# Kernel tuning notes

Measured on AMD Instinct MI355X. Metric: run time of the kernel, lower is better.

Reference implementation:

```python
import jax, jax.numpy as jnp
import numpy as np

N_EMBD = 1024
N_HEAD = 16
HEAD_DIM = N_EMBD // N_HEAD
B, T = 2, 2048


def setup_inputs() -> dict:
    key = jax.random.key(0)
    ks = jax.random.split(key, 9)
    s = 1.0 / np.sqrt(N_EMBD)
    return {
        "x": jax.random.normal(ks[0], (B, T, N_EMBD), dtype=jnp.float32),
        "Wq": jax.random.normal(ks[1], (N_EMBD, N_EMBD), dtype=jnp.float32) * s,
        "bq": jax.random.normal(ks[2], (N_EMBD,), dtype=jnp.float32) * s,
        "Wk": jax.random.normal(ks[3], (N_EMBD, N_EMBD), dtype=jnp.float32) * s,
        "bk": jax.random.normal(ks[4], (N_EMBD,), dtype=jnp.float32) * s,
        "Wv": jax.random.normal(ks[5], (N_EMBD, N_EMBD), dtype=jnp.float32) * s,
        "bv": jax.random.normal(ks[6], (N_EMBD,), dtype=jnp.float32) * s,
        "Wp": jax.random.normal(ks[7], (N_EMBD, N_EMBD), dtype=jnp.float32) * s,
        "bp": jax.random.normal(ks[8], (N_EMBD,), dtype=jnp.float32) * s,
    }


def reference(x, Wq, bq, Wk, bk, Wv, bv, Wp, bp):
    b, t, c = x.shape
    # torch Linear: y = x @ W.T + b
    def proj(W, bias):
        y = jnp.einsum('btc,oc->bto', x, W) + bias
        return y.reshape(b, t, N_HEAD, HEAD_DIM).transpose(0, 2, 1, 3)  # [B,H,T,D]

    q = proj(Wq, bq)
    k = proj(Wk, bk)
    v = proj(Wv, bv)

    scale = 1.0 / np.sqrt(HEAD_DIM).astype(np.float32)
    scores = jnp.einsum('bhqd,bhkd->bhqk', q, k) * scale  # [B,H,T,T]
    causal = jnp.tril(jnp.ones((t, t), dtype=bool))
    scores = jnp.where(causal[None, None], scores, jnp.float32(-jnp.inf))
    attn = jax.nn.softmax(scores, axis=-1)
    out = jnp.einsum('bhqk,bhkd->bhqd', attn, v)  # [B,H,T,D]
    out = out.transpose(0, 2, 1, 3).reshape(b, t, c)
    out = jnp.einsum('btc,oc->bto', out, Wp) + bp
    return out
```

## Files before the change

kernel.cpp:

```cpp
#include <hip/hip_runtime.h>
#include <hip/hip_bf16.h>

#define TT 2048
#define MM 4096

typedef __attribute__((ext_vector_type(8))) short bf16x8;
typedef __attribute__((ext_vector_type(4))) float f32x4;

__device__ inline short f2bf(float f){
  union { float f; unsigned u; } x; x.f = f;
  unsigned r = x.u + 0x7FFFu + ((x.u >> 16) & 1u);
  return (short)(r >> 16);
}
__device__ inline int pk2bf(float a, float b){
  __hip_bfloat162 h2 = __float22bfloat162_rn(make_float2(a, b));
  return *(int*)&h2;
}

__device__ inline void async16(const void* g, void* l){
  __builtin_amdgcn_global_load_lds((const __attribute__((address_space(1))) void*)g,
                                   (__attribute__((address_space(3))) void*)l, 16, 0, 0);
}

__global__ void cvt_all(const float* __restrict__ x,
                        const float* __restrict__ Wq, const float* __restrict__ Wk,
                        const float* __restrict__ Wv, const float* __restrict__ Wp,
                        short* __restrict__ xb, short* __restrict__ Wqb, short* __restrict__ Wkb,
                        short* __restrict__ Wvb, short* __restrict__ Wpb){
  int b = blockIdx.x;
  const float* in; short* out; int base;
  if (b < 4096)      { in = x;  out = xb;  base = b; }
  else if (b < 5120) { in = Wq; out = Wqb; base = b - 4096; }
  else if (b < 6144) { in = Wk; out = Wkb; base = b - 5120; }
  else if (b < 7168) { in = Wv; out = Wvb; base = b - 6144; }
  else               { in = Wp; out = Wpb; base = b - 7168; }
  int i = base * 256 + threadIdx.x;
  float4 v = ((const float4*)in)[i];
  short4 o;
  o.x = f2bf(v.x); o.y = f2bf(v.y); o.z = f2bf(v.z); o.w = f2bf(v.w);
  ((short4*)out)[i] = o;
}

__device__ inline void gemm_core(const short* __restrict__ A, const short* __restrict__ Wm,
                                 short* As, short* Bs, int m0, int n0,
                                 int tid, int wm, int wn, int quad, int lr,
                                 f32x4 acc[4][4])
{
  const int prow = tid >> 2, pcol = (tid & 3) << 3;
  const short* Ap0 = A  + (size_t)(m0 + prow) * 1024 + pcol;
  const short* Ap1 = A  + (size_t)(m0 + prow + 64) * 1024 + pcol;
  const short* Bp0 = Wm + (size_t)(n0 + prow) * 1024 + pcol;
  const short* Bp1 = Wm + (size_t)(n0 + prow + 64) * 1024 + pcol;
  for (int kt = 0; kt < 16; ++kt){
    const int kk = kt * 64;
#pragma unroll
    for (int pn = 0; pn < 2; ++pn){
      async16(Ap0 + kk + pn*32, As + pn*4096 + (size_t)tid * 8);
      async16(Ap1 + kk + pn*32, As + pn*4096 + (size_t)(tid + 256) * 8);
      async16(Bp0 + kk + pn*32, Bs + pn*4096 + (size_t)tid * 8);
      async16(Bp1 + kk + pn*32, Bs + pn*4096 + (size_t)(tid + 256) * 8);
    }
    __syncthreads();
#pragma unroll
    for (int ks = 0; ks < 2; ++ks){
      bf16x8 aF[4], bF[4];
#pragma unroll
      for (int mt = 0; mt < 4; ++mt) aF[mt] = *(const bf16x8*)(As + ks*4096 + (wm*64 + mt*16 + lr)*32 + quad*8);
#pragma unroll
      for (int nt = 0; nt < 4; ++nt) bF[nt] = *(const bf16x8*)(Bs + ks*4096 + (wn*64 + nt*16 + lr)*32 + quad*8);
#pragma unroll
      for (int mt = 0; mt < 4; ++mt)
#pragma unroll
        for (int nt = 0; nt < 4; ++nt)
          acc[mt][nt] = __builtin_amdgcn_mfma_f32_16x16x32_bf16(aF[mt], bF[nt], acc[mt][nt], 0, 0, 0);
    }
    __syncthreads();
  }
}

__launch_bounds__(256, 3)
__global__ void gemm_qkv(const short* __restrict__ A,
                         const short* __restrict__ W0, const short* __restrict__ W1, const short* __restrict__ W2,
                         const float* __restrict__ b0, const float* __restrict__ b1, const float* __restrict__ b2,
                         short* __restrict__ Qo, short* __restrict__ Ko, short* __restrict__ Vt)
{
  __shared__ __align__(16) short smem[16384];
  short* As = smem;
  short* Bs = smem + 8192;
  const int z = blockIdx.z;
  const short* Wm   = (z == 0) ? W0 : ((z == 1) ? W1 : W2);
  const float* bias = (z == 0) ? b0 : ((z == 1) ? b1 : b2);
  const int tid = threadIdx.x;
  const int lane = tid & 63, wave = tid >> 6;
  const int wm = wave >> 1, wn = wave & 1;
  const int quad = lane >> 4, lr = lane & 15;
  const int m0 = blockIdx.y * 128, n0 = blockIdx.x * 128;

  f32x4 acc[4][4];
#pragma unroll
  for (int i = 0; i < 4; ++i)
#pragma unroll
    for (int j = 0; j < 4; ++j)
#pragma unroll
      for (int r = 0; r < 4; ++r) acc[i][j][r] = 0.f;

  gemm_core(A, Wm, As, Bs, m0, n0, tid, wm, wn, quad, lr, acc);

  const float qscale = 0.125f * 1.4426950408889634f;
  const int bB = m0 >> 11, t0 = m0 & 2047;

  if (z == 2){
#pragma unroll
    for (int nh = 0; nh < 2; ++nh){
      __syncthreads();
      if (wn == nh){
#pragma unroll
        for (int nt = 0; nt < 4; ++nt){
          int n = n0 + wn*64 + nt*16 + lr;
          float bv = bias[n];
          int n_l = nt*16 + lr;
#pragma unroll
          for (int mt = 0; mt < 4; ++mt)
#pragma unroll
            for (int r = 0; r < 4; ++r){
              int m_l = wm*64 + mt*16 + quad*4 + r;
              smem[n_l*136 + m_l] = f2bf(acc[mt][nt][r] + bv);
            }
        }
      }
      __syncthreads();
#pragma unroll
      for (int i = 0; i < 4; ++i){
        int c = tid + i*256;
        int rowN = c >> 4, ch = c & 15;
        int4 v = *(const int4*)(smem + rowN*136 + ch*8);
        int n = n0 + nh*64 + rowN;
        int hH = n >> 6, d = n & 63;
        *(int4*)(Vt + ((size_t)((bB<<4) + hH)*64 + d)*2048 + t0 + ch*8) = v;
      }
    }
    return;
  }

  short* dst = (z == 0) ? Qo : Ko;
#pragma unroll
  for (int nh = 0; nh < 2; ++nh){
    __syncthreads();
    if (wn == nh){
#pragma unroll
      for (int nt = 0; nt < 4; ++nt){
        int n_l = nt*16 + lr;
        float bv = bias[n0 + nh*64 + n_l];
#pragma unroll
        for (int mt = 0; mt < 4; ++mt){
#pragma unroll
          for (int r = 0; r < 4; ++r){
            int m_l = wm*64 + mt*16 + quad*4 + r;
            float v = acc[mt][nt][r] + bv;
            if (z == 0) v *= qscale;
            smem[m_l*72 + n_l] = f2bf(v);
          }
        }
      }
    }
    __syncthreads();
    const int hH = (n0 + nh*64) >> 6;
    short* dhead = dst + (size_t)((bB<<4) + hH) * 2048 * 64;
#pragma unroll
    for (int i = 0; i < 4; ++i){
      int c = tid + i*256;
      int rowm = c >> 3, ch = (c & 7) << 3;
      int4 v = *(const int4*)(smem + rowm*72 + ch);
      *(int4*)(dhead + (size_t)(t0 + rowm)*64 + ch) = v;
    }
  }
}

__launch_bounds__(256, 2)
__global__ void gemm_proj(const short* __restrict__ A, const short* __restrict__ Wm,
                          const float* __restrict__ bias, float* __restrict__ out)
{
  __shared__ __align__(16) short As[2*4096];
  __shared__ __align__(16) short Bs[2*2048];
  const int tid = threadIdx.x;
  const int lane = tid & 63, wave = tid >> 6;
  const int quad = lane >> 4, lr = lane & 15;
  const int m0 = blockIdx.y * 128, n0 = blockIdx.x * 64;

  const int prow = tid >> 2, pcol = (tid & 3) << 3;
  const short* Ap0 = A  + (size_t)(m0 + prow) * 1024 + pcol;
  const short* Ap1 = A  + (size_t)(m0 + prow + 64) * 1024 + pcol;
  const short* Bp0 = Wm + (size_t)(n0 + (tid >> 2)) * 1024 + pcol;

  f32x4 acc[2][4];
#pragma unroll
  for (int i = 0; i < 2; ++i)
#pragma unroll
    for (int j = 0; j < 4; ++j)
#pragma unroll
      for (int r = 0; r < 4; ++r) acc[i][j][r] = 0.f;

  for (int kt = 0; kt < 16; ++kt){
    const int kk = kt * 64;
#pragma unroll
    for (int pn = 0; pn < 2; ++pn){
      async16(Ap0 + kk + pn*32, As + pn*4096 + (size_t)tid * 8);
      async16(Ap1 + kk + pn*32, As + pn*4096 + (size_t)(tid + 256) * 8);
      async16(Bp0 + kk + pn*32, Bs + pn*2048 + (size_t)tid * 8);
    }
    __syncthreads();
#pragma unroll
    for (int ks = 0; ks < 2; ++ks){
      bf16x8 aF[2], bF[4];
#pragma unroll
      for (int mt = 0; mt < 2; ++mt) aF[mt] = *(const bf16x8*)(As + ks*4096 + (wave*32 + mt*16 + lr)*32 + quad*8);
#pragma unroll
      for (int nt = 0; nt < 4; ++nt) bF[nt] = *(const bf16x8*)(Bs + ks*2048 + (nt*16 + lr)*32 + quad*8);
#pragma unroll
      for (int mt = 0; mt < 2; ++mt)
#pragma unroll
        for (int nt = 0; nt < 4; ++nt)
          acc[mt][nt] = __builtin_amdgcn_mfma_f32_16x16x32_bf16(aF[mt], bF[nt], acc[mt][nt], 0, 0, 0);
    }
    __syncthreads();
  }

#pragma unroll
  for (int nt = 0; nt < 4; ++nt){
    int n = n0 + nt*16 + lr;
    float bv = bias[n];
#pragma unroll
    for (int mt = 0; mt < 2; ++mt){
      int mBase = m0 + wave*32 + mt*16 + quad*4;
#pragma unroll
      for (int r = 0; r < 4; ++r){
        int m = mBase + r;
        out[(size_t)m * 1024 + n] = acc[mt][nt][r] + bv;
      }
    }
  }
}

__launch_bounds__(256, 2)
__global__ void attn_kernel(const short* __restrict__ Q, const short* __restrict__ K,
                            const short* __restrict__ Vt, short* __restrict__ AO)
{
  __shared__ __align__(16) short Ks[2][4096];
  __shared__ __align__(16) short Vs[2][4096];
  __shared__ __align__(16) short Ps[8192];
  const int tid = threadIdx.x, lane = tid & 63, wave = tid >> 6;
  const int quad = lane >> 4, lr = lane & 15;
  const int bid = blockIdx.x;
  const int pass = bid >> 8;
  const int a = (bid >> 5) & 7;
  const int hb = bid & 31;
  const int qb = pass ? a : (15 - a);
  const int bidx = hb >> 4, h = hb & 15;
  const int wq0 = qb * 128 + wave * 32;
  const short* Qh = Q  + (size_t)hb * TT * 64;
  const short* Kh = K  + (size_t)hb * TT * 64;
  const short* Vh = Vt + (size_t)hb * 64 * TT;
  short* Pw = Ps + wave * 2048;

  const int srow = tid >> 3;
  const int ssw  = (tid & 7) ^ (srow & 7);
  const short* Kp0 = Kh + (size_t)srow * 64 + ssw * 8;
  const short* Vp0 = Vh + (size_t)srow * TT + ssw * 8;

  bf16x8 qf[2][2];
#pragma unroll
  for (int g = 0; g < 2; ++g)
#pragma unroll
    for (int ks = 0; ks < 2; ++ks)
      qf[g][ks] = *(const bf16x8*)(Qh + (size_t)(wq0 + g*16 + lr) * 64 + ks*32 + quad*8);

  const int lsw0 = (((0*4 + quad) ^ (lr & 7)) << 3);
  const int lsw1 = (((1*4 + quad) ^ (lr & 7)) << 3);
  const int qh2 = quad >> 1, qlo = (quad & 1) << 2;

  f32x4 acc_o[2][4], l_acc[2];
#pragma unroll
  for (int g = 0; g < 2; ++g){
#pragma unroll
    for (int r = 0; r < 4; ++r) l_acc[g][r] = 0.f;
#pragma unroll
    for (int dt = 0; dt < 4; ++dt)
#pragma unroll
      for (int r = 0; r < 4; ++r) acc_o[g][dt][r] = 0.f;
  }

  const short one_bf = (short)0x3F80;
  const bf16x8 onesf = { one_bf, one_bf, one_bf, one_bf, one_bf, one_bf, one_bf, one_bf };

  const int nkv = 2*qb + 2;
  const int qtw = wq0 >> 6;
  async16(Kp0,           &Ks[0][(size_t)tid * 8]);
  async16(Kp0 + 32*64,   &Ks[0][(size_t)(tid + 256) * 8]);
  async16(Vp0,           &Vs[0][(size_t)tid * 8]);
  async16(Vp0 + 32*TT,   &Vs[0][(size_t)(tid + 256) * 8]);

  int cur = 0;
  for (int kv = 0; kv < nkv; ++kv){
    const int kv0 = kv * 64;
    __syncthreads();
    if (kv + 1 < nkv){
      const short* kp = Kp0 + (size_t)(kv + 1) * 4096;
      const short* vp = Vp0 + (kv + 1) * 64;
      const int nb = cur ^ 1;
      async16(kp,          &Ks[nb][(size_t)tid * 8]);
      async16(kp + 32*64,  &Ks[nb][(size_t)(tid + 256) * 8]);
      async16(vp,          &Vs[nb][(size_t)tid * 8]);
      async16(vp + 32*TT,  &Vs[nb][(size_t)(tid + 256) * 8]);
    }
    if (kv0 <= wq0 + 31){
      f32x4 s4[2][4];
#pragma unroll
      for (int g = 0; g < 2; ++g)
#pragma unroll
        for (int nt = 0; nt < 4; ++nt)
#pragma unroll
          for (int r = 0; r < 4; ++r) s4[g][nt][r] = 0.f;
#pragma unroll
      for (int nt = 0; nt < 4; ++nt){
        bf16x8 kf0 = *(const bf16x8*)(&Ks[cur][(nt*16 + lr)*64 + lsw0]);
        bf16x8 kf1 = *(const bf16x8*)(&Ks[cur][(nt*16 + lr)*64 + lsw1]);
#pragma unroll
        for (int g = 0; g < 2; ++g){
          s4[g][nt] = __builtin_amdgcn_mfma_f32_16x16x32_bf16(kf0, qf[g][0], s4[g][nt], 0, 0, 0);
          s4[g][nt] = __builtin_amdgcn_mfma_f32_16x16x32_bf16(kf1, qf[g][1], s4[g][nt], 0, 0, 0);
        }
      }

      const bool need_mask = (kv == qtw);
#pragma unroll
      for (int g = 0; g < 2; ++g){
        const int qglob = wq0 + g*16 + lr;
        short* Pg = Pw + g*1024;
#pragma unroll
        for (int nt = 0; nt < 4; ++nt){
          const int keyb = kv0 + nt*16 + quad*4;
          float pv[4];
#pragma unroll
          for (int r = 0; r < 4; ++r){
            float v = exp2f(s4[g][nt][r]);
            if (need_mask && keyb + r > qglob) v = 0.f;
            pv[r] = v;
          }
          int2 w;
          w.x = pk2bf(pv[0], pv[1]);
          w.y = pk2bf(pv[2], pv[3]);
          const int gg = nt*2 + qh2;
          *(int2*)(Pg + lr*64 + ((gg ^ (lr & 7)) << 3) + qlo) = w;
        }
      }

#pragma unroll
      for (int ks = 0; ks < 2; ++ks){
        const int lsw = ks ? lsw1 : lsw0;
        bf16x8 ptf0 = *(const bf16x8*)(Pw + lr*64 + lsw);
        bf16x8 ptf1 = *(const bf16x8*)(Pw + 1024 + lr*64 + lsw);
        l_acc[0] = __builtin_amdgcn_mfma_f32_16x16x32_bf16(onesf, ptf0, l_acc[0], 0, 0, 0);
        l_acc[1] = __builtin_amdgcn_mfma_f32_16x16x32_bf16(onesf, ptf1, l_acc[1], 0, 0, 0);
#pragma unroll
        for (int dt = 0; dt < 4; ++dt){
          bf16x8 vf = *(const bf16x8*)(&Vs[cur][(dt*16 + lr)*64 + lsw]);
          acc_o[0][dt] = __builtin_amdgcn_mfma_f32_16x16x32_bf16(vf, ptf0, acc_o[0][dt], 0, 0, 0);
          acc_o[1][dt] = __builtin_amdgcn_mfma_f32_16x16x32_bf16(vf, ptf1, acc_o[1][dt], 0, 0, 0);
        }
      }
    }
    cur ^= 1;
  }

#pragma unroll
  for (int g = 0; g < 2; ++g){
    short* Pg = Pw + g*1024;
    const float inv = __builtin_amdgcn_rcpf(l_acc[g][0]);
#pragma unroll
    for (int dt = 0; dt < 4; ++dt){
      int2 w;
      w.x = pk2bf(acc_o[g][dt][0] * inv, acc_o[g][dt][1] * inv);
      w.y = pk2bf(acc_o[g][dt][2] * inv, acc_o[g][dt][3] * inv);
      const int gg = dt*2 + qh2;
      *(int2*)(Pg + lr*64 + ((gg ^ (lr & 7)) << 3) + qlo) = w;
    }
#pragma unroll
    for (int i = 0; i < 2; ++i){
      int c = lane + i*64;
      int row = c >> 3, ch = c & 7;
      int4 v = *(const int4*)(Pg + row*64 + ((ch ^ (row & 7)) << 3));
      *(int4*)(AO + (size_t)(bidx*2048 + wq0 + g*16 + row)*1024 + h*64 + ch*8) = v;
    }
  }
}

extern "C" void kernel_launch(void* const* d_in, const int* in_sizes, int n_in,
                              void* d_out, int out_size, void* d_ws, size_t ws_size,
                              hipStream_t stream)
{
  const float* x  = (const float*)d_in[0];
  const float* Wq = (const float*)d_in[1];
  const float* bq = (const float*)d_in[2];
  const float* Wk = (const float*)d_in[3];
  const float* bk = (const float*)d_in[4];
  const float* Wv = (const float*)d_in[5];
  const float* bv = (const float*)d_in[6];
  const float* Wp = (const float*)d_in[7];
  const float* bp = (const float*)d_in[8];
  float* out = (float*)d_out;

  char* ws = (char*)d_ws;
  const size_t MB = 1024ull * 1024ull;
  short* Qb  = (short*)(ws + 0);
  short* Kb  = (short*)(ws + 8*MB);
  short* Vtb = (short*)(ws + 16*MB);
  short* AOb = (short*)(ws + 24*MB);
  short* xb  = (short*)(ws + 24*MB);
  short* Wqb = (short*)(ws + 32*MB);
  short* Wkb = (short*)(ws + 34*MB);
  short* Wvb = (short*)(ws + 36*MB);
  short* Wpb = (short*)(ws + 38*MB);

  cvt_all<<<8192, 256, 0, stream>>>(x, Wq, Wk, Wv, Wp, xb, Wqb, Wkb, Wvb, Wpb);
  gemm_qkv<<<dim3(8, 32, 3), 256, 0, stream>>>(xb, Wqb, Wkb, Wvb, bq, bk, bv, Qb, Kb, Vtb);
  attn_kernel<<<512, 256, 0, stream>>>(Qb, Kb, Vtb, AOb);
  gemm_proj<<<dim3(16, 32), 256, 0, stream>>>(AOb, Wpb, bp, out);
}
```

Baseline: 197.2 us.

## Split long causal attention query blocks across KV ranges with a combine kernel

Query blocks 8-15 are now split into two KV-range slices, assigned through a packed constant table, so attention runs as 768 balanced blocks instead of 512 unevenly sized ones. Split blocks write unnormalized fp32 partial outputs and row sums to workspace, and a new combine kernel adds the halves, normalizes, and writes bf16 output. Launch bounds rise to 3 blocks per SM to raise occupancy. The cost is extra fp32 global traffic, an added kernel launch, and possible register spilling under the tighter bound. The combine skips a max-rescale, which matches the existing kernel's softmax scheme.

Measured after the change: 187.0 us. -5.2%, faster.

```diff
diff --git a/kernel.cpp b/kernel.cpp
--- a/kernel.cpp
+++ b/kernel.cpp
@@ -241,9 +241,21 @@
   }
 }
 
-__launch_bounds__(256, 2)
+__device__ __constant__ int slice_tbl[24] = {
+  30736, 31760,     2,
+  14352, 26638,  2052,
+  28687, 24589,  4102,
+  29647, 20491,  6152,
+  27534, 18442,  8202,
+  25421, 10252, 16393,
+  12302, 21195, 16969,
+  22540, 23308, 19082
+};
+
+__launch_bounds__(256, 3)
 __global__ void attn_kernel(const short* __restrict__ Q, const short* __restrict__ K,
-                            const short* __restrict__ Vt, short* __restrict__ AO)
+                            const short* __restrict__ Vt, short* __restrict__ AO,
+                            float* __restrict__ Opart, float* __restrict__ Lpart)
 {
   __shared__ __align__(16) short Ks[2][4096];
   __shared__ __align__(16) short Vs[2][4096];
@@ -251,10 +263,13 @@
   const int tid = threadIdx.x, lane = tid & 63, wave = tid >> 6;
   const int quad = lane >> 4, lr = lane & 15;
   const int bid = blockIdx.x;
-  const int pass = bid >> 8;
   const int a = (bid >> 5) & 7;
   const int hb = bid & 31;
-  const int qb = pass ? a : (15 - a);
+  const int j = bid >> 8;
+  const int e = slice_tbl[a*3 + j];
+  const int qb = e >> 11, kv_s = (e >> 6) & 31, kvn = e & 63;
+  const bool split = (kvn != 2*qb + 2);
+  const int half = (kv_s != 0) ? 1 : 0;
   const int bidx = hb >> 4, h = hb & 15;
   const int wq0 = qb * 128 + wave * 32;
   const short* Qh = Q  + (size_t)hb * TT * 64;
@@ -292,18 +307,22 @@
   const short one_bf = (short)0x3F80;
   const bf16x8 onesf = { one_bf, one_bf, one_bf, one_bf, one_bf, one_bf, one_bf, one_bf };
 
-  const int nkv = 2*qb + 2;
+  const int kv_e = kv_s + kvn;
   const int qtw = wq0 >> 6;
-  async16(Kp0,           &Ks[0][(size_t)tid * 8]);
-  async16(Kp0 + 32*64,   &Ks[0][(size_t)(tid + 256) * 8]);
-  async16(Vp0,           &Vs[0][(size_t)tid * 8]);
-  async16(Vp0 + 32*TT,   &Vs[0][(size_t)(tid + 256) * 8]);
+  {
+    const short* kp = Kp0 + (size_t)kv_s * 4096;
+    const short* vp = Vp0 + kv_s * 64;
+    async16(kp,          &Ks[0][(size_t)tid * 8]);
+    async16(kp + 32*64,  &Ks[0][(size_t)(tid + 256) * 8]);
+    async16(vp,          &Vs[0][(size_t)tid * 8]);
+    async16(vp + 32*TT,  &Vs[0][(size_t)(tid + 256) * 8]);
+  }
 
   int cur = 0;
-  for (int kv = 0; kv < nkv; ++kv){
+  for (int kv = kv_s; kv < kv_e; ++kv){
     const int kv0 = kv * 64;
     __syncthreads();
-    if (kv + 1 < nkv){
+    if (kv + 1 < kv_e){
       const short* kp = Kp0 + (size_t)(kv + 1) * 4096;
       const short* vp = Vp0 + (kv + 1) * 64;
       const int nb = cur ^ 1;
@@ -372,6 +391,20 @@
     cur ^= 1;
   }
 
+  if (split){
+    const int p = (((hb << 3) | (qb - 8)) << 1) + half;
+    float* Op = Opart + (size_t)p * 8192;
+#pragma unroll
+    for (int g = 0; g < 2; ++g){
+      const int q_l = wave*32 + g*16 + lr;
+#pragma unroll
+      for (int dt = 0; dt < 4; ++dt)
+        *(f32x4*)(Op + q_l*64 + dt*16 + quad*4) = acc_o[g][dt];
+      if (lane < 16) Lpart[p*128 + wave*32 + g*16 + lane] = l_acc[g][0];
+    }
+    return;
+  }
+
 #pragma unroll
   for (int g = 0; g < 2; ++g){
     short* Pg = Pw + g*1024;
@@ -392,6 +425,25 @@
       *(int4*)(AO + (size_t)(bidx*2048 + wq0 + g*16 + row)*1024 + h*64 + ch*8) = v;
     }
   }
+}
+
+__global__ void attn_combine(const float* __restrict__ Opart, const float* __restrict__ Lpart,
+                             short* __restrict__ AO)
+{
+  const int gid = blockIdx.x * 256 + threadIdx.x;
+  const int row = gid >> 4, dq = (gid & 15) << 2;
+  const int hb = row >> 10, band = (row >> 7) & 7, r = row & 127;
+  const int p = ((hb << 3) | band) << 1;
+  const f32x4 a = *(const f32x4*)(Opart + (size_t)p*8192 + r*64 + dq);
+  const f32x4 b = *(const f32x4*)(Opart + (size_t)(p+1)*8192 + r*64 + dq);
+  const float l = Lpart[p*128 + r] + Lpart[(p+1)*128 + r];
+  const float inv = __builtin_amdgcn_rcpf(l);
+  int2 w;
+  w.x = pk2bf((a[0]+b[0])*inv, (a[1]+b[1])*inv);
+  w.y = pk2bf((a[2]+b[2])*inv, (a[3]+b[3])*inv);
+  const int t = (8 + band)*128 + r;
+  const int bidx = hb >> 4, h = hb & 15;
+  *(int2*)(AO + (size_t)(bidx*2048 + t)*1024 + h*64 + dq) = w;
 }
 
 extern "C" void kernel_launch(void* const* d_in, const int* in_sizes, int n_in,
@@ -420,9 +472,12 @@
   short* Wkb = (short*)(ws + 34*MB);
   short* Wvb = (short*)(ws + 36*MB);
   short* Wpb = (short*)(ws + 38*MB);
+  float* Opart = (float*)(ws + 40*MB);
+  float* Lpart = (float*)(ws + 56*MB);
 
   cvt_all<<<8192, 256, 0, stream>>>(x, Wq, Wk, Wv, Wp, xb, Wqb, Wkb, Wvb, Wpb);
   gemm_qkv<<<dim3(8, 32, 3), 256, 0, stream>>>(xb, Wqb, Wkb, Wvb, bq, bk, bv, Qb, Kb, Vtb);
-  attn_kernel<<<512, 256, 0, stream>>>(Qb, Kb, Vtb, AOb);
+  attn_kernel<<<768, 256, 0, stream>>>(Qb, Kb, Vtb, AOb, Opart, Lpart);
+  attn_combine<<<2048, 256, 0, stream>>>(Opart, Lpart, AOb);
   gemm_proj<<<dim3(16, 32), 256, 0, stream>>>(AOb, Wpb, bp, out);
 }
```
